# Kernel tuning notes

Hardware: AMD Instinct MI355X
Metric: run time of the kernel (lower is better)

The kernel has to match this reference:

```python
import jax, jax.numpy as jnp
import numpy as np

D = 1024          # embeddings_dims
HS = 128          # head_size = D // no_of_q_heads(=8)
NKV = 2           # hardcoded self.no_of_kv_heads = 2 (number of query Linear layers)


def apply_rope(x):
    # x: [..., T, d]; pairs of adjacent elements rotated (faithful to RotaryEmbeddings)
    d = x.shape[-1]
    T = x.shape[-2]
    positions = jnp.arange(0, d, 2, dtype=jnp.float32)           # step-2 positions (as in source)
    theta = 10000.0 ** (-2.0 * positions / d)                    # [d/2]
    angles = jnp.arange(T, dtype=jnp.float32)[:, None] * theta[None, :]  # [T, d/2]
    cos, sin = jnp.cos(angles), jnp.sin(angles)
    xr = x.reshape(x.shape[:-1] + (d // 2, 2))
    out = jnp.stack([xr[..., 0] * cos - xr[..., 1] * sin,
                     xr[..., 1] * cos + xr[..., 0] * sin], axis=-1)
    return out.reshape(x.shape)


def setup_inputs() -> dict:
    key = jax.random.key(0)
    k1, k2, k3, k4, k5 = jax.random.split(key, 5)
    B, T = 4, 2048
    x = jax.random.normal(k1, (B, T, D), dtype=jnp.float32)
    s = 1.0 / np.sqrt(D)
    Wq = jax.random.normal(k2, (NKV, HS, D), dtype=jnp.float32) * s  # 2 query Linear layers [out,in]
    Wk = jax.random.normal(k3, (HS, D), dtype=jnp.float32) * s
    Wv = jax.random.normal(k4, (HS, D), dtype=jnp.float32) * s
    Wo = jax.random.normal(k5, (D, NKV * HS), dtype=jnp.float32) * (1.0 / np.sqrt(NKV * HS))
    return {"x": x, "Wq": Wq, "Wk": Wk, "Wv": Wv, "Wo": Wo}


def reference(x, Wq, Wk, Wv, Wo):
    B, T, _ = x.shape
    k = apply_rope(x @ Wk.T)                              # [B,T,HS]
    v = x @ Wv.T                                          # [B,T,HS]
    q = jnp.einsum('btd,hkd->bhtk', x, Wq)                # [B,2,T,HS]
    q = apply_rope(q)
    scale = HS ** (-0.5)
    scores = jnp.einsum('bhtk,bsk->bhts', q, k) * scale   # [B,2,T,T]
    causal = jnp.tril(jnp.ones((T, T), dtype=bool))
    scores = jnp.where(causal, scores, -jnp.inf)
    w = jax.nn.softmax(scores, axis=-1)                   # dropout is identity at eval
    out = jnp.einsum('bhts,bsk->bhtk', w, v)              # [B,2,T,HS]
    out = out.transpose(0, 2, 1, 3).reshape(B, T, NKV * HS)  # concat heads on last dim
    return out @ Wo.T                                     # [B,T,D]
```

## Files before the change

kernel.cpp:

```cpp
#include <hip/hip_runtime.h>
#include <math.h>

#define DD 1024
#define HSZ 128
#define NB 4
#define TT 2048

typedef __attribute__((ext_vector_type(8))) short bf16x8;
typedef __attribute__((ext_vector_type(4))) float f32x4;

typedef __attribute__((address_space(3))) unsigned int lds_u32_t;
typedef __attribute__((address_space(1))) unsigned int glb_u32_t;

__device__ inline void gll16(const void* g, void* l) {
    __builtin_amdgcn_global_load_lds((const glb_u32_t*)g, (lds_u32_t*)l, 16, 0, 0);
}

__device__ inline unsigned short f2bf(float f){
    unsigned u = __builtin_bit_cast(unsigned, f);
    u += 0x7fff + ((u >> 16) & 1);
    return (unsigned short)(u >> 16);
}

__global__ __launch_bounds__(256) void prep_kernel(
    const float* __restrict__ Wq, const float* __restrict__ Wk,
    const float* __restrict__ Wv, const float* __restrict__ Wo,
    unsigned short* __restrict__ Wbp, unsigned short* __restrict__ Wop,
    float2* __restrict__ tab)
{
    int bid = blockIdx.x, tid = threadIdx.x;
    if (bid < 512) {
        int i = bid * 256 + tid;
        int t = i >> 6, j = i & 63;
        float theta = __powf(10000.f, -(float)j * (1.f / 32.f));
        float ang = (float)t * theta;
        tab[i] = make_float2(__cosf(ang), __sinf(ang));
        return;
    }
    const float* s;
    unsigned short* dst;
    if (bid < 768) {
        int gc = (bid - 512) * 256 + tid;
        int tileid = gc >> 10;
        int ct = tileid >> 4, kk = tileid & 15;
        int ch = gc & 1023;
        int ns = ch >> 7, kc = (ch >> 6) & 1, l6 = ch & 63;
        int wrow = ct * 128 + ns * 16 + (l6 & 15);
        int kcol = kk * 64 + kc * 32 + (l6 >> 4) * 8;
        s = (wrow < 256) ? Wq + (size_t)wrow * DD
          : (wrow < 384) ? Wk + (size_t)(wrow - 256) * DD
                         : Wv + (size_t)(wrow - 384) * DD;
        s += kcol;
        dst = Wbp + (size_t)gc * 8;
    } else {
        int gc = (bid - 768) * 256 + tid;
        int tileid = gc >> 10;
        int ct = tileid >> 2, kk = tileid & 3;
        int ch = gc & 1023;
        int ns = ch >> 7, kc = (ch >> 6) & 1, l6 = ch & 63;
        int orow = ct * 128 + ns * 16 + (l6 & 15);
        int kcol = kk * 64 + kc * 32 + (l6 >> 4) * 8;
        s = Wo + (size_t)orow * 256 + kcol;
        dst = Wop + (size_t)gc * 8;
    }
    float4 a = ((const float4*)s)[0];
    float4 c = ((const float4*)s)[1];
    unsigned short o[8] = {f2bf(a.x),f2bf(a.y),f2bf(a.z),f2bf(a.w),
                           f2bf(c.x),f2bf(c.y),f2bf(c.z),f2bf(c.w)};
    *(uint4*)dst = *(const uint4*)o;
}

__global__ __launch_bounds__(256) void qkv_gemm_kernel(
    const float* __restrict__ x,
    const unsigned short* __restrict__ Wbp,
    const float2* __restrict__ tab,
    unsigned short* __restrict__ qo,
    unsigned short* __restrict__ Kp,
    unsigned short* __restrict__ Vp)
{
    int bid = blockIdx.x;
    int rt = bid & 127, ct = bid >> 7;
    int row0 = rt * 64;
    int b = row0 >> 11, t0 = row0 & (TT - 1);
    int tid = threadIdx.x;
    int wave = tid >> 6, lane = tid & 63;
    int mrow = lane & 15, quad = lane >> 4;

    __shared__ unsigned short Bs[2][8192];

    f32x4 acc[8];
    #pragma unroll
    for (int ns = 0; ns < 8; ++ns)
        #pragma unroll
        for (int r = 0; r < 4; ++r) acc[ns][r] = 0.f;

    const float* xrow = x + (size_t)(row0 + wave * 16 + mrow) * DD;

    {
        const unsigned short* wt = Wbp + (size_t)(ct * 16) * 8192;
        #pragma unroll
        for (int u = 0; u < 4; ++u)
            gll16(wt + (size_t)(u * 256 + tid) * 8, &Bs[0][(u * 256 + (tid & 192)) * 8]);
    }

    for (int kk = 0; kk < 16; ++kk) {
        __syncthreads();
        if (kk < 15) {
            const unsigned short* wt = Wbp + (size_t)(ct * 16 + kk + 1) * 8192;
            #pragma unroll
            for (int u = 0; u < 4; ++u)
                gll16(wt + (size_t)(u * 256 + tid) * 8, &Bs[(kk + 1) & 1][(u * 256 + (tid & 192)) * 8]);
        }
        bf16x8 af[2];
        #pragma unroll
        for (int kc = 0; kc < 2; ++kc) {
            const float* s = xrow + kk * 64 + kc * 32 + quad * 8;
            float4 f0 = ((const float4*)s)[0];
            float4 f1 = ((const float4*)s)[1];
            bf16x8 pk;
            pk[0]=(short)f2bf(f0.x); pk[1]=(short)f2bf(f0.y); pk[2]=(short)f2bf(f0.z); pk[3]=(short)f2bf(f0.w);
            pk[4]=(short)f2bf(f1.x); pk[5]=(short)f2bf(f1.y); pk[6]=(short)f2bf(f1.z); pk[7]=(short)f2bf(f1.w);
            af[kc] = pk;
        }
        const unsigned short* Bcur = Bs[kk & 1];
        #pragma unroll
        for (int kc = 0; kc < 2; ++kc)
            #pragma unroll
            for (int ns = 0; ns < 8; ++ns) {
                bf16x8 bb = *(const bf16x8*)(Bcur + ((ns * 2 + kc) * 64 + lane) * 8);
                acc[ns] = __builtin_amdgcn_mfma_f32_16x16x32_bf16(af[kc], bb, acc[ns], 0, 0, 0);
            }
    }

    __syncthreads();

    if (ct < 2) {
        unsigned short* dst = qo + (size_t)(b * 2 + ct) * TT * HSZ;
        #pragma unroll
        for (int ns = 0; ns < 8; ++ns) {
            int colloc = ns * 16 + mrow;
            int pj = colloc >> 1;
            #pragma unroll
            for (int r = 0; r < 4; ++r) {
                int t = t0 + wave * 16 + quad * 4 + r;
                float v = acc[ns][r];
                float vp = __shfl_xor(v, 1, 64);
                float2 cs = tab[t * 64 + pj];
                float outv = ((mrow & 1) == 0) ? (v * cs.x - vp * cs.y)
                                               : (v * cs.x + vp * cs.y);
                dst[(size_t)t * HSZ + colloc] = f2bf(outv);
            }
        }
    } else if (ct == 2) {
        unsigned short* A_ = (unsigned short*)Bs;
        #pragma unroll
        for (int ns = 0; ns < 8; ++ns) {
            int colloc = ns * 16 + mrow;
            int pj = colloc >> 1;
            int chunk = (ns >> 1) * 4 + wave;
            int lph = (ns & 1) * 2 + (mrow >> 3);
            #pragma unroll
            for (int r = 0; r < 4; ++r) {
                int t = t0 + wave * 16 + quad * 4 + r;
                float v = acc[ns][r];
                float vp = __shfl_xor(v, 1, 64);
                float2 cs = tab[t * 64 + pj];
                float outv = ((mrow & 1) == 0) ? (v * cs.x - vp * cs.y)
                                               : (v * cs.x + vp * cs.y);
                A_[chunk * 512 + (lph * 16 + quad * 4 + r) * 8 + (mrow & 7)] = f2bf(outv);
            }
        }
        __syncthreads();
        unsigned short* kd = Kp + (size_t)(b * 32 + (t0 >> 6)) * 8192;
        #pragma unroll
        for (int u = 0; u < 4; ++u)
            *(uint4*)(kd + (u * 256 + tid) * 8) = *(const uint4*)(A_ + (u * 256 + tid) * 8);
    } else {
        unsigned short* A_ = (unsigned short*)Bs;
        #pragma unroll
        for (int ns = 0; ns < 8; ++ns) {
            int chunk = ns * 2 + (wave >> 1);
            int lanep = ((wave & 1) * 2 + (quad >> 1)) * 16 + mrow;
            #pragma unroll
            for (int r = 0; r < 4; ++r)
                A_[chunk * 512 + lanep * 8 + (quad & 1) * 4 + r] = f2bf(acc[ns][r]);
        }
        __syncthreads();
        unsigned short* vd = Vp + (size_t)(b * 32 + (t0 >> 6)) * 8192;
        #pragma unroll
        for (int u = 0; u < 4; ++u)
            *(uint4*)(vd + (u * 256 + tid) * 8) = *(const uint4*)(A_ + (u * 256 + tid) * 8);
    }
}

__global__ __launch_bounds__(256) void attn_mfma_kernel(
    const unsigned short* __restrict__ q,
    const unsigned short* __restrict__ Kp,
    const unsigned short* __restrict__ Vp,
    unsigned short* __restrict__ att)
{
    int bid = blockIdx.x;
    int rr = bid >> 3;
    int qt = (rr < 32) ? rr : 63 - (rr - 32);
    int bh = bid & 7;
    int b = bh >> 1, h = bh & 1;
    int q0 = qt * 32;
    int tid = threadIdx.x;
    int wave = tid >> 6, lane = tid & 63;
    int qsub = wave >> 1, par = wave & 1;
    int qw0 = q0 + qsub * 16;
    int mrow = lane & 15, quad = lane >> 4;

    __shared__ char raw[74240];
    unsigned short* Ks0 = (unsigned short*)raw;
    unsigned short* Vs0 = (unsigned short*)(raw + 32768);
    unsigned short* Psb = (unsigned short*)(raw + 65536);
    float* Ms_ = (float*)(raw + 73728);
    float* Ls_ = Ms_ + 32;
    float* Os  = (float*)raw;

    const unsigned short* qrow = q + (((size_t)(b * 2 + h)) * TT + qw0 + mrow) * HSZ + quad * 8;
    bf16x8 qf[4];
    #pragma unroll
    for (int c = 0; c < 4; ++c) qf[c] = *(const bf16x8*)(qrow + 32 * c);

    float mrun[4], lrun[4];
    f32x4 O[8];
    #pragma unroll
    for (int r = 0; r < 4; ++r) { mrun[r] = -1e30f; lrun[r] = 0.f; }
    #pragma unroll
    for (int g = 0; g < 8; ++g)
        #pragma unroll
        for (int r = 0; r < 4; ++r) O[g][r] = 0.f;

    const int NT = (qt + 2) >> 1;
    const float scl = 0.08838834764831845f;

    for (int jj = 0; jj < NT; jj += 2) {
        __syncthreads();
        for (int tp = 0; tp < 2; ++tp) {
            int j = jj + tp;
            if (j >= NT) break;
            const unsigned short* ks = Kp + (size_t)(b * 32 + j) * 8192;
            const unsigned short* vs = Vp + (size_t)(b * 32 + j) * 8192;
            #pragma unroll
            for (int u = 0; u < 4; ++u) {
                gll16(ks + (size_t)(u * 256 + tid) * 8, Ks0 + (tp * 8192) + (u * 256 + (tid & 192)) * 8);
                gll16(vs + (size_t)(u * 256 + tid) * 8, Vs0 + (tp * 8192) + (u * 256 + (tid & 192)) * 8);
            }
        }
        __syncthreads();

        int j = jj + par;
        int s0 = j * 64;
        if (j < NT && s0 <= qw0 + 15) {
            const unsigned short* Kt = Ks0 + par * 8192;
            const unsigned short* Vtt = Vs0 + par * 8192;

            f32x4 S[4];
            #pragma unroll
            for (int f = 0; f < 4; ++f)
                #pragma unroll
                for (int r = 0; r < 4; ++r) S[f][r] = 0.f;

            #pragma unroll
            for (int c = 0; c < 4; ++c)
                #pragma unroll
                for (int f = 0; f < 4; ++f) {
                    bf16x8 bk = *(const bf16x8*)(Kt + ((c * 4 + f) * 64 + lane) * 8);
                    S[f] = __builtin_amdgcn_mfma_f32_16x16x32_bf16(qf[c], bk, S[f], 0, 0, 0);
                }

            #pragma unroll
            for (int f = 0; f < 4; ++f) {
                int sg = s0 + 16 * f + mrow;
                #pragma unroll
                for (int r = 0; r < 4; ++r) {
                    int qg = qw0 + quad * 4 + r;
                    float val = S[f][r] * scl;
                    S[f][r] = (sg <= qg) ? val : -1e30f;
                }
            }

            float al[4];
            #pragma unroll
            for (int r = 0; r < 4; ++r) {
                float v = fmaxf(fmaxf(S[0][r], S[1][r]), fmaxf(S[2][r], S[3][r]));
                v = fmaxf(v, __shfl_xor(v, 1, 64));
                v = fmaxf(v, __shfl_xor(v, 2, 64));
                v = fmaxf(v, __shfl_xor(v, 4, 64));
                v = fmaxf(v, __shfl_xor(v, 8, 64));
                float mn = fmaxf(mrun[r], v);
                al[r] = __expf(mrun[r] - mn);
                mrun[r] = mn;
            }
            #pragma unroll
            for (int f = 0; f < 4; ++f)
                #pragma unroll
                for (int r = 0; r < 4; ++r)
                    S[f][r] = __expf(S[f][r] - mrun[r]);
            #pragma unroll
            for (int r = 0; r < 4; ++r) {
                float v = (S[0][r] + S[1][r]) + (S[2][r] + S[3][r]);
                v += __shfl_xor(v, 1, 64);
                v += __shfl_xor(v, 2, 64);
                v += __shfl_xor(v, 4, 64);
                v += __shfl_xor(v, 8, 64);
                lrun[r] = lrun[r] * al[r] + v;
            }
            #pragma unroll
            for (int g = 0; g < 8; ++g) {
                O[g][0] *= al[0]; O[g][1] *= al[1]; O[g][2] *= al[2]; O[g][3] *= al[3];
            }

            unsigned short* Pw = Psb + wave * 1024;
            #pragma unroll
            for (int f = 0; f < 4; ++f) {
                int p = f >> 1;
                int hi2 = (2 * f + (mrow >> 3)) & 3;
                int jlo = mrow & 7;
                #pragma unroll
                for (int r = 0; r < 4; ++r)
                    Pw[(p * 64 + hi2 * 16 + quad * 4 + r) * 8 + jlo] = f2bf(S[f][r]);
            }
            bf16x8 pa[2];
            pa[0] = *(const bf16x8*)(Pw + lane * 8);
            pa[1] = *(const bf16x8*)(Pw + (64 + lane) * 8);

            #pragma unroll
            for (int g = 0; g < 8; ++g)
                #pragma unroll
                for (int p = 0; p < 2; ++p) {
                    bf16x8 bv = *(const bf16x8*)(Vtt + ((g * 2 + p) * 64 + lane) * 8);
                    O[g] = __builtin_amdgcn_mfma_f32_16x16x32_bf16(pa[p], bv, O[g], 0, 0, 0);
                }
        }
    }

    __syncthreads();
    if (par == 1) {
        if (mrow == 0) {
            #pragma unroll
            for (int r = 0; r < 4; ++r) {
                Ms_[qsub * 16 + quad * 4 + r] = mrun[r];
                Ls_[qsub * 16 + quad * 4 + r] = lrun[r];
            }
        }
        float* Ow = Os + qsub * 2048;
        #pragma unroll
        for (int g = 0; g < 8; ++g)
            #pragma unroll
            for (int r = 0; r < 4; ++r)
                Ow[(quad * 4 + r) * 128 + g * 16 + mrow] = O[g][r];
    }
    __syncthreads();
    if (par == 0) {
        const float* Op = Os + qsub * 2048;
        float A0[4], A1[4], inv[4];
        #pragma unroll
        for (int r = 0; r < 4; ++r) {
            float m1 = Ms_[qsub * 16 + quad * 4 + r];
            float l1 = Ls_[qsub * 16 + quad * 4 + r];
            float m12 = fmaxf(mrun[r], m1);
            A0[r] = __expf(mrun[r] - m12);
            A1[r] = __expf(m1 - m12);
            inv[r] = 1.f / (lrun[r] * A0[r] + l1 * A1[r]);
        }
        unsigned short* ab = att + (((size_t)b * TT + qw0) * 2 + h) * 128;
        #pragma unroll
        for (int g = 0; g < 8; ++g)
            #pragma unroll
            for (int r = 0; r < 4; ++r) {
                int row = quad * 4 + r;
                float o = (O[g][r] * A0[r] + Op[row * 128 + g * 16 + mrow] * A1[r]) * inv[r];
                ab[(size_t)row * 256 + g * 16 + mrow] = f2bf(o);
            }
    }
}

__global__ __launch_bounds__(256) void outproj_gemm_kernel(
    const unsigned short* __restrict__ attb,
    const unsigned short* __restrict__ Wop,
    float* __restrict__ y)
{
    int bid = blockIdx.x;
    int rt = bid & 127, ct = bid >> 7;
    int row0 = rt * 64;
    int tid = threadIdx.x;
    int wave = tid >> 6, lane = tid & 63;
    int mrow = lane & 15, quad = lane >> 4;

    __shared__ unsigned short Bs[2][8192];

    f32x4 acc[8];
    #pragma unroll
    for (int ns = 0; ns < 8; ++ns)
        #pragma unroll
        for (int r = 0; r < 4; ++r) acc[ns][r] = 0.f;

    const unsigned short* arow = attb + (size_t)(row0 + wave * 16 + mrow) * 256;

    {
        const unsigned short* wt = Wop + (size_t)(ct * 4) * 8192;
        #pragma unroll
        for (int u = 0; u < 4; ++u)
            gll16(wt + (size_t)(u * 256 + tid) * 8, &Bs[0][(u * 256 + (tid & 192)) * 8]);
    }

    for (int kk = 0; kk < 4; ++kk) {
        __syncthreads();
        if (kk < 3) {
            const unsigned short* wt = Wop + (size_t)(ct * 4 + kk + 1) * 8192;
            #pragma unroll
            for (int u = 0; u < 4; ++u)
                gll16(wt + (size_t)(u * 256 + tid) * 8, &Bs[(kk + 1) & 1][(u * 256 + (tid & 192)) * 8]);
        }
        const unsigned short* Bcur = Bs[kk & 1];
        #pragma unroll
        for (int kc = 0; kc < 2; ++kc) {
            bf16x8 af = *(const bf16x8*)(arow + kk * 64 + kc * 32 + quad * 8);
            #pragma unroll
            for (int ns = 0; ns < 8; ++ns) {
                bf16x8 bb = *(const bf16x8*)(Bcur + ((ns * 2 + kc) * 64 + lane) * 8);
                acc[ns] = __builtin_amdgcn_mfma_f32_16x16x32_bf16(af, bb, acc[ns], 0, 0, 0);
            }
        }
    }

    #pragma unroll
    for (int ns = 0; ns < 8; ++ns)
        #pragma unroll
        for (int r = 0; r < 4; ++r) {
            int row = row0 + wave * 16 + quad * 4 + r;
            y[(size_t)row * DD + ct * 128 + ns * 16 + mrow] = acc[ns][r];
        }
}

extern "C" void kernel_launch(void* const* d_in, const int* in_sizes, int n_in,
                              void* d_out, int out_size, void* d_ws, size_t ws_size,
                              hipStream_t stream) {
    const float* x  = (const float*)d_in[0];
    const float* Wq = (const float*)d_in[1];
    const float* Wk = (const float*)d_in[2];
    const float* Wv = (const float*)d_in[3];
    const float* Wo = (const float*)d_in[4];
    float* y = (float*)d_out;

    char* ws = (char*)d_ws;
    unsigned short* at  = (unsigned short*)(ws);
    unsigned short* qo  = (unsigned short*)(ws + 4u  * 1024 * 1024);
    unsigned short* Kp  = (unsigned short*)(ws + 8u  * 1024 * 1024);
    unsigned short* Vp  = (unsigned short*)(ws + 10u * 1024 * 1024);
    unsigned short* Wbp = (unsigned short*)(ws + 12u * 1024 * 1024);
    unsigned short* Wop = (unsigned short*)(ws + 13u * 1024 * 1024);
    float2*         tb  = (float2*)        (ws + 13824u * 1024);

    prep_kernel<<<896, 256, 0, stream>>>(Wq, Wk, Wv, Wo, Wbp, Wop, tb);
    qkv_gemm_kernel<<<512, 256, 0, stream>>>(x, Wbp, tb, qo, Kp, Vp);
    attn_mfma_kernel<<<512, 256, 0, stream>>>(qo, Kp, Vp, at);
    outproj_gemm_kernel<<<1024, 256, 0, stream>>>(at, Wop, y);
}
```

Before: 167.4 us.

## Retile QKV and out-projection GEMMs to 128-row tiles; use exp2 in softmax

Measured after the change: 191.2 us. +14.2%, slower.

```diff
diff --git a/kernel.cpp b/kernel.cpp
--- a/kernel.cpp
+++ b/kernel.cpp
@@ -41,11 +41,11 @@
     unsigned short* dst;
     if (bid < 768) {
         int gc = (bid - 512) * 256 + tid;
-        int tileid = gc >> 10;
+        int tileid = gc >> 9;
         int ct = tileid >> 4, kk = tileid & 15;
-        int ch = gc & 1023;
+        int ch = gc & 511;
         int ns = ch >> 7, kc = (ch >> 6) & 1, l6 = ch & 63;
-        int wrow = ct * 128 + ns * 16 + (l6 & 15);
+        int wrow = ct * 64 + ns * 16 + (l6 & 15);
         int kcol = kk * 64 + kc * 32 + (l6 >> 4) * 8;
         s = (wrow < 256) ? Wq + (size_t)wrow * DD
           : (wrow < 384) ? Wk + (size_t)(wrow - 256) * DD
@@ -79,117 +79,149 @@
     unsigned short* __restrict__ Vp)
 {
     int bid = blockIdx.x;
-    int rt = bid & 127, ct = bid >> 7;
-    int row0 = rt * 64;
+    int rt = bid >> 3, ct = bid & 7;
+    int row0 = rt * 128;
     int b = row0 >> 11, t0 = row0 & (TT - 1);
     int tid = threadIdx.x;
     int wave = tid >> 6, lane = tid & 63;
     int mrow = lane & 15, quad = lane >> 4;
 
-    __shared__ unsigned short Bs[2][8192];
-
-    f32x4 acc[8];
+    __shared__ unsigned short Bs[2][4096];
+
+    f32x4 acc[2][4];
     #pragma unroll
-    for (int ns = 0; ns < 8; ++ns)
-        #pragma unroll
-        for (int r = 0; r < 4; ++r) acc[ns][r] = 0.f;
-
-    const float* xrow = x + (size_t)(row0 + wave * 16 + mrow) * DD;
+    for (int rs = 0; rs < 2; ++rs)
+        #pragma unroll
+        for (int ns = 0; ns < 4; ++ns)
+            #pragma unroll
+            for (int r = 0; r < 4; ++r) acc[rs][ns][r] = 0.f;
+
+    const float* xr0 = x + (size_t)(row0 + wave * 32 + mrow) * DD;
+    const float* xr1 = xr0 + 16 * DD;
 
     {
-        const unsigned short* wt = Wbp + (size_t)(ct * 16) * 8192;
-        #pragma unroll
-        for (int u = 0; u < 4; ++u)
-            gll16(wt + (size_t)(u * 256 + tid) * 8, &Bs[0][(u * 256 + (tid & 192)) * 8]);
+        const unsigned short* wt = Wbp + (size_t)(ct * 16) * 4096;
+        gll16(wt + (size_t)(tid) * 8,        &Bs[0][((tid & 192)) * 8]);
+        gll16(wt + (size_t)(256 + tid) * 8,  &Bs[0][(256 + (tid & 192)) * 8]);
     }
 
     for (int kk = 0; kk < 16; ++kk) {
         __syncthreads();
         if (kk < 15) {
-            const unsigned short* wt = Wbp + (size_t)(ct * 16 + kk + 1) * 8192;
-            #pragma unroll
-            for (int u = 0; u < 4; ++u)
-                gll16(wt + (size_t)(u * 256 + tid) * 8, &Bs[(kk + 1) & 1][(u * 256 + (tid & 192)) * 8]);
-        }
-        bf16x8 af[2];
-        #pragma unroll
-        for (int kc = 0; kc < 2; ++kc) {
-            const float* s = xrow + kk * 64 + kc * 32 + quad * 8;
-            float4 f0 = ((const float4*)s)[0];
-            float4 f1 = ((const float4*)s)[1];
-            bf16x8 pk;
-            pk[0]=(short)f2bf(f0.x); pk[1]=(short)f2bf(f0.y); pk[2]=(short)f2bf(f0.z); pk[3]=(short)f2bf(f0.w);
-            pk[4]=(short)f2bf(f1.x); pk[5]=(short)f2bf(f1.y); pk[6]=(short)f2bf(f1.z); pk[7]=(short)f2bf(f1.w);
-            af[kc] = pk;
-        }
-        const unsigned short* Bcur = Bs[kk & 1];
+            const unsigned short* wt = Wbp + (size_t)(ct * 16 + kk + 1) * 4096;
+            unsigned short* bnext = Bs[(kk + 1) & 1];
+            gll16(wt + (size_t)(tid) * 8,       bnext + ((tid & 192)) * 8);
+            gll16(wt + (size_t)(256 + tid) * 8, bnext + (256 + (tid & 192)) * 8);
+        }
+        bf16x8 af[2][2];
+        #pragma unroll
+        for (int rs = 0; rs < 2; ++rs)
+            #pragma unroll
+            for (int kc = 0; kc < 2; ++kc) {
+                const float* s = (rs ? xr1 : xr0) + kk * 64 + kc * 32 + quad * 8;
+                float4 f0 = ((const float4*)s)[0];
+                float4 f1 = ((const float4*)s)[1];
+                bf16x8 pk;
+                pk[0]=(short)f2bf(f0.x); pk[1]=(short)f2bf(f0.y); pk[2]=(short)f2bf(f0.z); pk[3]=(short)f2bf(f0.w);
+                pk[4]=(short)f2bf(f1.x); pk[5]=(short)f2bf(f1.y); pk[6]=(short)f2bf(f1.z); pk[7]=(short)f2bf(f1.w);
+                af[rs][kc] = pk;
+            }
+        const unsigned short* Bc = Bs[kk & 1];
         #pragma unroll
         for (int kc = 0; kc < 2; ++kc)
             #pragma unroll
-            for (int ns = 0; ns < 8; ++ns) {
-                bf16x8 bb = *(const bf16x8*)(Bcur + ((ns * 2 + kc) * 64 + lane) * 8);
-                acc[ns] = __builtin_amdgcn_mfma_f32_16x16x32_bf16(af[kc], bb, acc[ns], 0, 0, 0);
+            for (int ns = 0; ns < 4; ++ns) {
+                bf16x8 bb = *(const bf16x8*)(Bc + ((ns * 2 + kc) * 64 + lane) * 8);
+                #pragma unroll
+                for (int rs = 0; rs < 2; ++rs)
+                    acc[rs][ns] = __builtin_amdgcn_mfma_f32_16x16x32_bf16(af[rs][kc], bb, acc[rs][ns], 0, 0, 0);
             }
     }
 
     __syncthreads();
 
-    if (ct < 2) {
-        unsigned short* dst = qo + (size_t)(b * 2 + ct) * TT * HSZ;
-        #pragma unroll
-        for (int ns = 0; ns < 8; ++ns) {
-            int colloc = ns * 16 + mrow;
-            int pj = colloc >> 1;
-            #pragma unroll
-            for (int r = 0; r < 4; ++r) {
-                int t = t0 + wave * 16 + quad * 4 + r;
-                float v = acc[ns][r];
-                float vp = __shfl_xor(v, 1, 64);
-                float2 cs = tab[t * 64 + pj];
-                float outv = ((mrow & 1) == 0) ? (v * cs.x - vp * cs.y)
-                                               : (v * cs.x + vp * cs.y);
-                dst[(size_t)t * HSZ + colloc] = f2bf(outv);
-            }
-        }
-    } else if (ct == 2) {
-        unsigned short* A_ = (unsigned short*)Bs;
-        #pragma unroll
-        for (int ns = 0; ns < 8; ++ns) {
-            int colloc = ns * 16 + mrow;
-            int pj = colloc >> 1;
-            int chunk = (ns >> 1) * 4 + wave;
-            int lph = (ns & 1) * 2 + (mrow >> 3);
-            #pragma unroll
-            for (int r = 0; r < 4; ++r) {
-                int t = t0 + wave * 16 + quad * 4 + r;
-                float v = acc[ns][r];
-                float vp = __shfl_xor(v, 1, 64);
-                float2 cs = tab[t * 64 + pj];
-                float outv = ((mrow & 1) == 0) ? (v * cs.x - vp * cs.y)
-                                               : (v * cs.x + vp * cs.y);
-                A_[chunk * 512 + (lph * 16 + quad * 4 + r) * 8 + (mrow & 7)] = f2bf(outv);
+    if (ct < 4) {
+        int h = ct >> 1;
+        int cbase = (ct & 1) * 64;
+        unsigned short* dst = qo + (size_t)(b * 2 + h) * TT * HSZ;
+        #pragma unroll
+        for (int rs = 0; rs < 2; ++rs)
+            #pragma unroll
+            for (int ns = 0; ns < 4; ++ns) {
+                int colloc = cbase + ns * 16 + mrow;
+                int pj = colloc >> 1;
+                #pragma unroll
+                for (int r = 0; r < 4; ++r) {
+                    int t = t0 + wave * 32 + rs * 16 + quad * 4 + r;
+                    float v = acc[rs][ns][r];
+                    float vp = __shfl_xor(v, 1, 64);
+                    float2 cs = tab[t * 64 + pj];
+                    float outv = ((mrow & 1) == 0) ? (v * cs.x - vp * cs.y)
+                                                   : (v * cs.x + vp * cs.y);
+                    dst[(size_t)t * HSZ + colloc] = f2bf(outv);
+                }
+            }
+    } else if (ct < 6) {
+        unsigned short* A_ = &Bs[0][0];
+        int dhalf = ct - 4;
+        #pragma unroll
+        for (int rs = 0; rs < 2; ++rs) {
+            int vw = wave * 2 + rs;
+            int kt = vw >> 2, f = vw & 3;
+            #pragma unroll
+            for (int ns = 0; ns < 4; ++ns) {
+                int d = dhalf * 64 + ns * 16 + mrow;
+                int c2 = ns >> 1;
+                int hi = (ns & 1) * 2 + (mrow >> 3);
+                int pj = d >> 1;
+                int lch = ((kt * 2 + c2) * 4 + f) * 64 + hi * 16;
+                #pragma unroll
+                for (int r = 0; r < 4; ++r) {
+                    int t = t0 + wave * 32 + rs * 16 + quad * 4 + r;
+                    float v = acc[rs][ns][r];
+                    float vp = __shfl_xor(v, 1, 64);
+                    float2 cs = tab[t * 64 + pj];
+                    float outv = ((mrow & 1) == 0) ? (v * cs.x - vp * cs.y)
+                                                   : (v * cs.x + vp * cs.y);
+                    A_[(lch + quad * 4 + r) * 8 + (mrow & 7)] = f2bf(outv);
+                }
             }
         }
         __syncthreads();
-        unsigned short* kd = Kp + (size_t)(b * 32 + (t0 >> 6)) * 8192;
-        #pragma unroll
-        for (int u = 0; u < 4; ++u)
-            *(uint4*)(kd + (u * 256 + tid) * 8) = *(const uint4*)(A_ + (u * 256 + tid) * 8);
+        #pragma unroll
+        for (int u = 0; u < 4; ++u) {
+            int ch = u * 256 + tid;
+            int kt = ch >> 9, c2 = (ch >> 8) & 1, rest = ch & 255;
+            int gch = (dhalf * 2 + c2) * 256 + rest;
+            unsigned short* kd = Kp + (size_t)(b * 32 + (t0 >> 6) + kt) * 8192;
+            *(uint4*)(kd + gch * 8) = *(const uint4*)(A_ + ch * 8);
+        }
     } else {
-        unsigned short* A_ = (unsigned short*)Bs;
-        #pragma unroll
-        for (int ns = 0; ns < 8; ++ns) {
-            int chunk = ns * 2 + (wave >> 1);
-            int lanep = ((wave & 1) * 2 + (quad >> 1)) * 16 + mrow;
-            #pragma unroll
-            for (int r = 0; r < 4; ++r)
-                A_[chunk * 512 + lanep * 8 + (quad & 1) * 4 + r] = f2bf(acc[ns][r]);
+        unsigned short* A_ = &Bs[0][0];
+        int dhalf = ct - 6;
+        #pragma unroll
+        for (int rs = 0; rs < 2; ++rs) {
+            int vw = wave * 2 + rs;
+            int kt = vw >> 2, p = (vw >> 1) & 1;
+            int lphi = (vw & 1) * 2 + (quad >> 1);
+            int j0 = (quad & 1) * 4;
+            #pragma unroll
+            for (int ns = 0; ns < 4; ++ns) {
+                int lch = ((kt * 4 + ns) * 2 + p) * 64 + lphi * 16 + mrow;
+                #pragma unroll
+                for (int r = 0; r < 4; ++r)
+                    A_[lch * 8 + j0 + r] = f2bf(acc[rs][ns][r]);
+            }
         }
         __syncthreads();
-        unsigned short* vd = Vp + (size_t)(b * 32 + (t0 >> 6)) * 8192;
-        #pragma unroll
-        for (int u = 0; u < 4; ++u)
-            *(uint4*)(vd + (u * 256 + tid) * 8) = *(const uint4*)(A_ + (u * 256 + tid) * 8);
+        #pragma unroll
+        for (int u = 0; u < 4; ++u) {
+            int ch = u * 256 + tid;
+            int kt = ch >> 9, rest = ch & 511;
+            int gch = dhalf * 512 + rest;
+            unsigned short* vd = Vp + (size_t)(b * 32 + (t0 >> 6) + kt) * 8192;
+            *(uint4*)(vd + gch * 8) = *(const uint4*)(A_ + ch * 8);
+        }
     }
 }
 
@@ -234,7 +266,7 @@
         for (int r = 0; r < 4; ++r) O[g][r] = 0.f;
 
     const int NT = (qt + 2) >> 1;
-    const float scl = 0.08838834764831845f;
+    const float s2l = 0.08838834764831845f * 1.4426950408889634f;
 
     for (int jj = 0; jj < NT; jj += 2) {
         __syncthreads();
@@ -277,7 +309,7 @@
                 #pragma unroll
                 for (int r = 0; r < 4; ++r) {
                     int qg = qw0 + quad * 4 + r;
-                    float val = S[f][r] * scl;
+                    float val = S[f][r] * s2l;
                     S[f][r] = (sg <= qg) ? val : -1e30f;
                 }
             }
@@ -291,14 +323,14 @@
                 v = fmaxf(v, __shfl_xor(v, 4, 64));
                 v = fmaxf(v, __shfl_xor(v, 8, 64));
                 float mn = fmaxf(mrun[r], v);
-                al[r] = __expf(mrun[r] - mn);
+                al[r] = exp2f(mrun[r] - mn);
                 mrun[r] = mn;
             }
             #pragma unroll
             for (int f = 0; f < 4; ++f)
                 #pragma unroll
                 for (int r = 0; r < 4; ++r)
-                    S[f][r] = __expf(S[f][r] - mrun[r]);
+                    S[f][r] = exp2f(S[f][r] - mrun[r]);
             #pragma unroll
             for (int r = 0; r < 4; ++r) {
                 float v = (S[0][r] + S[1][r]) + (S[2][r] + S[3][r]);
@@ -362,8 +394,8 @@
             float m1 = Ms_[qsub * 16 + quad * 4 + r];
             float l1 = Ls_[qsub * 16 + quad * 4 + r];
             float m12 = fmaxf(mrun[r], m1);
-            A0[r] = __expf(mrun[r] - m12);
-            A1[r] = __expf(m1 - m12);
+            A0[r] = exp2f(mrun[r] - m12);
+            A1[r] = exp2f(m1 - m12);
             inv[r] = 1.f / (lrun[r] * A0[r] + l1 * A1[r]);
         }
         unsigned short* ab = att + (((size_t)b * TT + qw0) * 2 + h) * 128;
@@ -384,21 +416,24 @@
     float* __restrict__ y)
 {
     int bid = blockIdx.x;
-    int rt = bid & 127, ct = bid >> 7;
-    int row0 = rt * 64;
+    int rt = bid >> 3, ct = bid & 7;
+    int row0 = rt * 128;
     int tid = threadIdx.x;
     int wave = tid >> 6, lane = tid & 63;
     int mrow = lane & 15, quad = lane >> 4;
 
     __shared__ unsigned short Bs[2][8192];
 
-    f32x4 acc[8];
+    f32x4 acc[2][8];
     #pragma unroll
-    for (int ns = 0; ns < 8; ++ns)
-        #pragma unroll
-        for (int r = 0; r < 4; ++r) acc[ns][r] = 0.f;
-
-    const unsigned short* arow = attb + (size_t)(row0 + wave * 16 + mrow) * 256;
+    for (int rs = 0; rs < 2; ++rs)
+        #pragma unroll
+        for (int ns = 0; ns < 8; ++ns)
+            #pragma unroll
+            for (int r = 0; r < 4; ++r) acc[rs][ns][r] = 0.f;
+
+    const unsigned short* ar0 = attb + (size_t)(row0 + wave * 32 + mrow) * 256;
+    const unsigned short* ar1 = ar0 + 16 * 256;
 
     {
         const unsigned short* wt = Wop + (size_t)(ct * 4) * 8192;
@@ -415,25 +450,29 @@
             for (int u = 0; u < 4; ++u)
                 gll16(wt + (size_t)(u * 256 + tid) * 8, &Bs[(kk + 1) & 1][(u * 256 + (tid & 192)) * 8]);
         }
-        const unsigned short* Bcur = Bs[kk & 1];
+        const unsigned short* Bc = Bs[kk & 1];
         #pragma unroll
         for (int kc = 0; kc < 2; ++kc) {
-            bf16x8 af = *(const bf16x8*)(arow + kk * 64 + kc * 32 + quad * 8);
+            bf16x8 af0 = *(const bf16x8*)(ar0 + kk * 64 + kc * 32 + quad * 8);
+            bf16x8 af1 = *(const bf16x8*)(ar1 + kk * 64 + kc * 32 + quad * 8);
             #pragma unroll
             for (int ns = 0; ns < 8; ++ns) {
-                bf16x8 bb = *(const bf16x8*)(Bcur + ((ns * 2 + kc) * 64 + lane) * 8);
-                acc[ns] = __builtin_amdgcn_mfma_f32_16x16x32_bf16(af, bb, acc[ns], 0, 0, 0);
+                bf16x8 bb = *(const bf16x8*)(Bc + ((ns * 2 + kc) * 64 + lane) * 8);
+                acc[0][ns] = __builtin_amdgcn_mfma_f32_16x16x32_bf16(af0, bb, acc[0][ns], 0, 0, 0);
+                acc[1][ns] = __builtin_amdgcn_mfma_f32_16x16x32_bf16(af1, bb, acc[1][ns], 0, 0, 0);
             }
         }
     }
 
     #pragma unroll
-    for (int ns = 0; ns < 8; ++ns)
-        #pragma unroll
-        for (int r = 0; r < 4; ++r) {
-            int row = row0 + wave * 16 + quad * 4 + r;
-            y[(size_t)row * DD + ct * 128 + ns * 16 + mrow] = acc[ns][r];
-        }
+    for (int rs = 0; rs < 2; ++rs)
+        #pragma unroll
+        for (int ns = 0; ns < 8; ++ns)
+            #pragma unroll
+            for (int r = 0; r < 4; ++r) {
+                int row = row0 + wave * 32 + rs * 16 + quad * 4 + r;
+                y[(size_t)row * DD + ct * 128 + ns * 16 + mrow] = acc[rs][ns][r];
+            }
 }
 
 extern "C" void kernel_launch(void* const* d_in, const int* in_sizes, int n_in,
@@ -458,5 +497,5 @@
     prep_kernel<<<896, 256, 0, stream>>>(Wq, Wk, Wv, Wo, Wbp, Wop, tb);
     qkv_gemm_kernel<<<512, 256, 0, stream>>>(x, Wbp, tb, qo, Kp, Vp);
     attn_mfma_kernel<<<512, 256, 0, stream>>>(qo, Kp, Vp, at);
-    outproj_gemm_kernel<<<1024, 256, 0, stream>>>(at, Wop, y);
-}
+    outproj_gemm_kernel<<<512, 256, 0, stream>>>(at, Wop, y);
+}
```
